# Kernel optimization log

Hardware: AMD Instinct MI355X
Metric: run time of the kernel (lower is better)

## Reference

```python
import jax, jax.numpy as jnp
import numpy as np

NH = 8  # num_heads
CHUNK = 32  # query-block size for chunked L1 cdist


def _mlp(x, w1, b1, w2, b2, w3, b3):
    h = jax.nn.relu(x @ w1 + b1)
    h = jax.nn.relu(h @ w2 + b2)
    return h @ w3 + b3


def _split_heads(x, nh):
    # Faithful to source: reshape last dim as (d, nh) then permute -> [B, nh, S, d]
    B, S, H = x.shape
    return jnp.transpose(x.reshape(B, S, H // nh, nh), (0, 3, 1, 2))


def _cdist_l1(K, Q, chunk=CHUNK):
    # torch.cdist(K, Q, p=1): D[b,h,i,j] = sum_d |K[b,h,i,d] - Q[b,h,j,d]|
    # Chunk over query rows to bound the broadcasted |K-Q| intermediate.
    B, h, Sq, d = Q.shape
    Sk = K.shape[2]
    Qb = jnp.moveaxis(Q.reshape(B, h, Sq // chunk, chunk, d), 2, 0)  # [nb,B,h,chunk,d]

    def block(q):  # q: [B,h,chunk,d]
        return jnp.sum(jnp.abs(K[:, :, :, None, :] - q[:, :, None, :, :]), axis=-1)  # [B,h,Sk,chunk]

    D = jax.lax.map(block, Qb)  # [nb,B,h,Sk,chunk]
    return jnp.moveaxis(D, 0, 3).reshape(B, h, Sk, Sq)


def setup_inputs() -> dict:
    key = jax.random.key(0)
    ks = jax.random.split(key, 32)
    B, S, F, H, O = 4, 1024, 128, 512, 128
    s = 0.02

    def lin(i, fin, fout):
        return (jax.random.normal(ks[i], (fin, fout), jnp.float32) * s,
                jnp.zeros((fout,), jnp.float32))

    inp = {
        'KEY': jax.random.normal(ks[0], (B, S, F), jnp.float32),
        'VALUE': jax.random.normal(ks[1], (B, S, F), jnp.float32),
        'QUERY': jax.random.normal(ks[2], (B, S, F), jnp.float32),
    }
    idx = 3
    for n in ['k', 'q', 'v']:
        for li, (fin, fout) in enumerate([(F, H), (H, H), (H, H)], 1):
            w, b = lin(idx, fin, fout); idx += 1
            inp[f'W{n}_w{li}'] = w
            inp[f'W{n}_b{li}'] = b
    w, b = lin(idx, H, O)
    inp['Wo_w'] = w
    inp['Wo_b'] = b
    return inp


def reference(KEY, VALUE, QUERY,
              Wk_w1, Wk_b1, Wk_w2, Wk_b2, Wk_w3, Wk_b3,
              Wq_w1, Wq_b1, Wq_w2, Wq_b2, Wq_w3, Wq_b3,
              Wv_w1, Wv_b1, Wv_w2, Wv_b2, Wv_w3, Wv_b3,
              Wo_w, Wo_b):
    Wk = _split_heads(_mlp(KEY, Wk_w1, Wk_b1, Wk_w2, Wk_b2, Wk_w3, Wk_b3), NH)   # [B,h,Sk,d]
    Wq = _split_heads(_mlp(QUERY, Wq_w1, Wq_b1, Wq_w2, Wq_b2, Wq_w3, Wq_b3), NH)  # [B,h,Sq,d]
    Wv = _split_heads(_mlp(VALUE, Wv_w1, Wv_b1, Wv_w2, Wv_b2, Wv_w3, Wv_b3), NH)  # [B,h,Sk,d]

    D = _cdist_l1(Wk, Wq)                              # [B,h,Sk,Sq]
    attn = jax.nn.softmax(-(D * D) * 0.5, axis=1)      # softmax over HEAD axis, as in source
    out = jnp.einsum('bhik,bhij->bhjk', attn, Wv)      # [B,h,d,Sq]
    B, h, d, Sq = out.shape
    out = jnp.transpose(out, (0, 2, 1, 3)).reshape(B, d * h, Sq)  # [B,hidden,Sq]
    out = jnp.transpose(out, (0, 2, 1))                # [B,Sq,hidden]
    return out @ Wo_w + Wo_b                           # dropout = identity (eval)
```

## Files before the change

kernel.cpp:

```cpp
#include <hip/hip_runtime.h>
#include <hip/hip_bf16.h>
#include <hip/hip_fp16.h>

typedef unsigned short u16;
typedef __attribute__((ext_vector_type(8))) short short8;
typedef __attribute__((ext_vector_type(4))) float floatx4;

#define DEVI static __device__ __forceinline__

DEVI float bf2f(u16 b) { return __uint_as_float(((unsigned)b) << 16); }
DEVI u16 f2bf(float f) {
  __hip_bfloat16 h = __float2bfloat16(f);
  u16 u; __builtin_memcpy(&u, &h, 2); return u;
}
DEVI u16 f2h(float f) {
  __half h = __float2half(f);
  u16 u; __builtin_memcpy(&u, &h, 2); return u;
}

DEVI void async_ld16(const u16* g, u16* l) {
  __builtin_amdgcn_global_load_lds(
      (const __attribute__((address_space(1))) unsigned int*)g,
      (__attribute__((address_space(3))) unsigned int*)l, 16, 0, 0);
}

template <int CTRL>
DEVI float dpp_add_f(float v) {
  int i; __builtin_memcpy(&i, &v, 4);
  int p = __builtin_amdgcn_update_dpp(0, i, CTRL, 0xF, 0xF, false);
  float pv; __builtin_memcpy(&pv, &p, 4);
  return v + pv;
}

DEVI int hperm(int f) { return ((f & 7) << 6) | (f >> 3); }

struct H4 { __half2 a, b, c, d; };
DEVI H4 toH4(const int4 v) { H4 r; __builtin_memcpy(&r, &v, 16); return r; }
DEVI int4 fromH4(const H4 x) { int4 r; __builtin_memcpy(&r, &x, 16); return r; }

struct TransArgs {
  const float* src[10];
  u16* dst[10];
  int R[10];
  int C[10];
};

__global__ __launch_bounds__(256) void transpose_k(TransArgs t) {
  const int z = blockIdx.z;
  const float* __restrict__ src = t.src[z];
  u16* __restrict__ dst = t.dst[z];
  const int R = t.R[z], C = t.C[z];
  const int c0 = blockIdx.x * 32, r0 = blockIdx.y * 32;
  if (c0 >= C || r0 >= R) return;
  __shared__ float tile[32][33];
  const int tx = threadIdx.x & 31, ty = threadIdx.x >> 5;
  for (int i = ty; i < 32; i += 8)
    tile[i][tx] = src[(size_t)(r0 + i) * C + c0 + tx];
  __syncthreads();
  for (int i = ty; i < 32; i += 8) {
    const int f = r0 + tx;
    const int fi = (z == 9) ? hperm(f) : f;
    dst[(size_t)(c0 + i) * R + fi] = f2bf(tile[tx][i]);
  }
}

struct ConvArgs {
  const float* src[3];
  u16* dst[3];
};

__global__ __launch_bounds__(256) void conv_k(ConvArgs c) {
  const int z = blockIdx.z;
  const float* __restrict__ src = c.src[z];
  u16* __restrict__ dst = c.dst[z];
  const size_t i = ((size_t)blockIdx.x * 256 + threadIdx.x) * 8;
  const float4 f0 = *(const float4*)(src + i);
  const float4 f1 = *(const float4*)(src + i + 4);
  u16 tmp[8] = {f2bf(f0.x), f2bf(f0.y), f2bf(f0.z), f2bf(f0.w),
                f2bf(f1.x), f2bf(f1.y), f2bf(f1.z), f2bf(f1.w)};
  int4 t; __builtin_memcpy(&t, tmp, 16);
  *(int4*)(dst + i) = t;
}

struct GemmArgs {
  const u16* A[3];
  const u16* WT[3];
  const float* bias[3];
  void* C[3];
};

__global__ __launch_bounds__(256, 3) void gemm128(GemmArgs ga, int M, int N, int K,
                                                  int relu, int c_mode, int out_perm) {
  const int z = blockIdx.z;
  const u16* __restrict__ A = ga.A[z];
  const u16* __restrict__ WT = ga.WT[z];
  const float* __restrict__ bias = ga.bias[z];
  void* __restrict__ C = ga.C[z];

  __shared__ u16 As[128 * 64];
  __shared__ u16 Bs[128 * 64];

  const int tid = threadIdx.x;
  const int lane = tid & 63;
  const int wave = tid >> 6;
  const int wm = wave >> 1, wn = wave & 1;
  const int mb = blockIdx.y, nb = blockIdx.x;

  floatx4 acc[4][4];
#pragma unroll
  for (int mi = 0; mi < 4; ++mi)
#pragma unroll
    for (int ni = 0; ni < 4; ++ni) acc[mi][ni] = floatx4{0.f, 0.f, 0.f, 0.f};

  const int g = (lane & 7) ^ ((lane >> 3) & 7);
  const int srow = lane >> 3;
  const size_t aRowBase = (size_t)(mb * 128 + wave * 32 + srow) * K + g * 8;
  const size_t bRowBase = (size_t)(nb * 128 + wave * 32 + srow) * K + g * 8;

  for (int k0 = 0; k0 < K; k0 += 64) {
    __syncthreads();
#pragma unroll
    for (int it = 0; it < 4; ++it) {
      async_ld16(A + aRowBase + (size_t)it * 8 * K + k0, As + (wave * 32 + it * 8) * 64);
      async_ld16(WT + bRowBase + (size_t)it * 8 * K + k0, Bs + (wave * 32 + it * 8) * 64);
    }
    __syncthreads();
#pragma unroll
    for (int ks = 0; ks < 2; ++ks) {
      const int phys = ((ks * 4 + (lane >> 4)) ^ (lane & 7)) * 8;
      short8 af[4], bf[4];
#pragma unroll
      for (int i = 0; i < 4; ++i) {
        const int m = wm * 64 + i * 16 + (lane & 15);
        const int n = wn * 64 + i * 16 + (lane & 15);
        af[i] = *(const short8*)(As + m * 64 + phys);
        bf[i] = *(const short8*)(Bs + n * 64 + phys);
      }
#pragma unroll
      for (int mi = 0; mi < 4; ++mi)
#pragma unroll
        for (int ni = 0; ni < 4; ++ni)
          acc[mi][ni] = __builtin_amdgcn_mfma_f32_16x16x32_bf16(af[mi], bf[ni], acc[mi][ni], 0, 0, 0);
    }
  }

#pragma unroll
  for (int mi = 0; mi < 4; ++mi)
#pragma unroll
    for (int ni = 0; ni < 4; ++ni) {
      const int col = nb * 128 + wn * 64 + ni * 16 + (lane & 15);
      const float bv = bias[col];
      const int colw = out_perm ? hperm(col) : col;
      const floatx4 v = acc[mi][ni];
#pragma unroll
      for (int r = 0; r < 4; ++r) {
        const int row = mb * 128 + wm * 64 + mi * 16 + (lane >> 4) * 4 + r;
        float x = v[r] + bv;
        if (relu) x = fmaxf(x, 0.f);
        if (c_mode == 1)      ((float*)C)[(size_t)row * N + colw] = x;
        else if (c_mode == 2) ((u16*)C)[(size_t)row * N + colw] = f2h(x);
        else                  ((u16*)C)[(size_t)row * N + colw] = f2bf(x);
      }
    }
}

__global__ __launch_bounds__(256, 4) void attn_kernel(const u16* __restrict__ Km,
                                                      const u16* __restrict__ Qm,
                                                      const u16* __restrict__ Vm,
                                                      u16* __restrict__ partial) {
  __shared__ alignas(16) u16 lds[4 * 2048];

  const int tid = threadIdx.x;
  const int lane = tid & 63;
  const int wave = tid >> 6;
  const int wid = blockIdx.x * 4 + wave;
  const int qt = wid & 127;
  const int sp = (wid >> 7) & 15;
  const int b = wid >> 11;
  const int j0 = qt * 8;

  const int qg = lane >> 4;
  const int h = (lane >> 1) & 7;
  const int half = lane & 1;

  int grans[4];
#pragma unroll
  for (int pi = 0; pi < 4; ++pi)
    grans[pi] = h * 8 + half * 4 + ((pi + h) & 3);

  H4 Qh[2][4];
#pragma unroll
  for (int qi = 0; qi < 2; ++qi) {
    const u16* qrow = Qm + (size_t)(b * 1024 + j0 + qg + qi * 4) * 512;
#pragma unroll
    for (int pi = 0; pi < 4; ++pi)
      Qh[qi][pi] = toH4(*(const int4*)(qrow + grans[pi] * 8));
  }

  const __half2 z2 = __float2half2_rn(0.f);
  H4 o[2][4];
#pragma unroll
  for (int qi = 0; qi < 2; ++qi)
#pragma unroll
    for (int pi = 0; pi < 4; ++pi) { o[qi][pi].a = z2; o[qi][pi].b = z2; o[qi][pi].c = z2; o[qi][pi].d = z2; }

  const int keyBase = b * 1024 + sp * 64;
  const u16* kbase = Km + (size_t)keyBase * 512;
  const u16* vbase = Vm + (size_t)keyBase * 512;

#pragma unroll 1
  for (int t = 0; t < 64; ++t) {
    const u16* krow = kbase + t * 512;
    const u16* vrow = vbase + t * 512;
    int4 kvi[4], vvi[4];
#pragma unroll
    for (int pi = 0; pi < 4; ++pi) {
      kvi[pi] = *(const int4*)(krow + grans[pi] * 8);
      vvi[pi] = *(const int4*)(vrow + grans[pi] * 8);
    }

    __half2 a0[2], a1[2];
    a0[0] = z2; a1[0] = z2; a0[1] = z2; a1[1] = z2;
#pragma unroll
    for (int pi = 0; pi < 4; ++pi) {
      const H4 k4 = toH4(kvi[pi]);
#pragma unroll
      for (int qi = 0; qi < 2; ++qi) {
        a0[qi] = __hadd2(a0[qi], __habs2(__hsub2(k4.a, Qh[qi][pi].a)));
        a1[qi] = __hadd2(a1[qi], __habs2(__hsub2(k4.b, Qh[qi][pi].b)));
        a0[qi] = __hadd2(a0[qi], __habs2(__hsub2(k4.c, Qh[qi][pi].c)));
        a1[qi] = __hadd2(a1[qi], __habs2(__hsub2(k4.d, Qh[qi][pi].d)));
      }
    }

    __half2 wh[2];
#pragma unroll
    for (int qi = 0; qi < 2; ++qi) {
      const __half2 s2 = __hadd2(a0[qi], a1[qi]);
      float d8p = __half2float(__low2half(s2)) + __half2float(__high2half(s2));
      const float d8 = dpp_add_f<0xB1>(d8p);
      const float e = __expf(-0.5f * d8 * d8);
      float nrm = e;
      nrm = dpp_add_f<0x4E>(nrm);
      nrm = dpp_add_f<0x141>(nrm);
      nrm = dpp_add_f<0x140>(nrm);
      const float w = e * __builtin_amdgcn_rcpf(nrm);
      wh[qi] = __float2half2_rn(w);
    }

#pragma unroll
    for (int pi = 0; pi < 4; ++pi) {
      const H4 v4 = toH4(vvi[pi]);
#pragma unroll
      for (int qi = 0; qi < 2; ++qi) {
        o[qi][pi].a = __hfma2(wh[qi], v4.a, o[qi][pi].a);
        o[qi][pi].b = __hfma2(wh[qi], v4.b, o[qi][pi].b);
        o[qi][pi].c = __hfma2(wh[qi], v4.c, o[qi][pi].c);
        o[qi][pi].d = __hfma2(wh[qi], v4.d, o[qi][pi].d);
      }
    }
  }

  u16* Ew = lds + wave * 2048;
#pragma unroll
  for (int qi = 0; qi < 2; ++qi) {
#pragma unroll
    for (int pi = 0; pi < 4; ++pi)
      *(int4*)(Ew + qg * 512 + grans[pi] * 8) = fromH4(o[qi][pi]);
    asm volatile("s_waitcnt lgkmcnt(0)" ::: "memory");
#pragma unroll
    for (int p = 0; p < 4; ++p) {
      const int4 v = *(const int4*)(Ew + p * 512 + lane * 8);
      u16* dst = partial + (size_t)sp * (4096 * 512) + (size_t)(b * 1024 + j0 + p + qi * 4) * 512;
      *(int4*)(dst + lane * 8) = v;
    }
    asm volatile("s_waitcnt lgkmcnt(0)" ::: "memory");
  }
}

__global__ __launch_bounds__(256) void reduce_k(const u16* __restrict__ p,
                                                u16* __restrict__ out) {
  const size_t i = ((size_t)blockIdx.x * 256 + threadIdx.x) * 8;
  float s[8] = {0.f, 0.f, 0.f, 0.f, 0.f, 0.f, 0.f, 0.f};
#pragma unroll
  for (int sp = 0; sp < 16; ++sp) {
    const int4 t = *(const int4*)(p + (size_t)sp * (4096 * 512) + i);
    const __half* th = reinterpret_cast<const __half*>(&t);
#pragma unroll
    for (int j = 0; j < 8; ++j) s[j] += __half2float(th[j]);
  }
  int4 pk;
  u16* pu = reinterpret_cast<u16*>(&pk);
#pragma unroll
  for (int j = 0; j < 8; ++j) pu[j] = f2bf(s[j]);
  *(int4*)(out + i) = pk;
}

extern "C" void kernel_launch(void* const* d_in, const int* in_sizes, int n_in,
                              void* d_out, int out_size, void* d_ws, size_t ws_size,
                              hipStream_t stream) {
  (void)in_sizes; (void)n_in; (void)out_size; (void)ws_size;
  char* wsp = (char*)d_ws;
  size_t off = 0;
  auto take = [&](size_t bytes) {
    void* p = (void*)(wsp + off);
    off += ((bytes + 255) & ~(size_t)255);
    return p;
  };

  static const int wR[10] = {128, 512, 512, 128, 512, 512, 128, 512, 512, 512};
  static const int wC[10] = {512, 512, 512, 512, 512, 512, 512, 512, 512, 128};
  static const int widx[10] = {3, 5, 7, 9, 11, 13, 15, 17, 19, 21};

  u16* WT[10];
  for (int i = 0; i < 10; ++i) WT[i] = (u16*)take((size_t)wR[i] * wC[i] * 2);
  u16* a0[3]; for (int i = 0; i < 3; ++i) a0[i] = (u16*)take((size_t)4096 * 128 * 2);
  u16* h1[3]; for (int i = 0; i < 3; ++i) h1[i] = (u16*)take((size_t)4096 * 512 * 2);
  u16* h2[3]; for (int i = 0; i < 3; ++i) h2[i] = (u16*)take((size_t)4096 * 512 * 2);
  u16* partial = (u16*)take((size_t)16 * 4096 * 512 * 2);

  TransArgs ta;
  for (int i = 0; i < 10; ++i) {
    ta.src[i] = (const float*)d_in[widx[i]];
    ta.dst[i] = WT[i];
    ta.R[i] = wR[i];
    ta.C[i] = wC[i];
  }
  hipLaunchKernelGGL(transpose_k, dim3(16, 16, 10), dim3(256), 0, stream, ta);

  ConvArgs ca;
  ca.src[0] = (const float*)d_in[0]; ca.src[1] = (const float*)d_in[2]; ca.src[2] = (const float*)d_in[1];
  ca.dst[0] = a0[0]; ca.dst[1] = a0[1]; ca.dst[2] = a0[2];
  hipLaunchKernelGGL(conv_k, dim3(256, 1, 3), dim3(256), 0, stream, ca);

  GemmArgs g1 = {};
  for (int i = 0; i < 3; ++i) g1.A[i] = a0[i];
  g1.WT[0] = WT[0]; g1.WT[1] = WT[3]; g1.WT[2] = WT[6];
  g1.bias[0] = (const float*)d_in[4]; g1.bias[1] = (const float*)d_in[10]; g1.bias[2] = (const float*)d_in[16];
  g1.C[0] = h1[0]; g1.C[1] = h1[1]; g1.C[2] = h1[2];
  hipLaunchKernelGGL(gemm128, dim3(4, 32, 3), dim3(256), 0, stream, g1, 4096, 512, 128, 1, 0, 0);

  GemmArgs g2 = {};
  for (int i = 0; i < 3; ++i) { g2.A[i] = h1[i]; g2.C[i] = h2[i]; }
  g2.WT[0] = WT[1]; g2.WT[1] = WT[4]; g2.WT[2] = WT[7];
  g2.bias[0] = (const float*)d_in[6]; g2.bias[1] = (const float*)d_in[12]; g2.bias[2] = (const float*)d_in[18];
  hipLaunchKernelGGL(gemm128, dim3(4, 32, 3), dim3(256), 0, stream, g2, 4096, 512, 512, 1, 0, 0);

  GemmArgs g3 = {};
  for (int i = 0; i < 3; ++i) { g3.A[i] = h2[i]; g3.C[i] = (void*)h1[i]; }
  g3.WT[0] = WT[2]; g3.WT[1] = WT[5]; g3.WT[2] = WT[8];
  g3.bias[0] = (const float*)d_in[8]; g3.bias[1] = (const float*)d_in[14]; g3.bias[2] = (const float*)d_in[20];
  hipLaunchKernelGGL(gemm128, dim3(4, 32, 3), dim3(256), 0, stream, g3, 4096, 512, 512, 0, 2, 1);

  hipLaunchKernelGGL(attn_kernel, dim3(2048), dim3(256), 0, stream, h1[0], h1[1], h1[2], partial);

  hipLaunchKernelGGL(reduce_k, dim3(1024), dim3(256), 0, stream, partial, h2[0]);

  GemmArgs g4 = {};
  g4.A[0] = h2[0]; g4.WT[0] = WT[9]; g4.bias[0] = (const float*)d_in[22]; g4.C[0] = d_out;
  hipLaunchKernelGGL(gemm128, dim3(1, 32, 1), dim3(256), 0, stream, g4, 4096, 128, 512, 0, 1, 0);
}
```

Before: 424.3 us.

## Double-buffer K/V rows into LDS with async global-to-LDS loads

The attention kernel now streams K and V rows into a per-wave double-buffered LDS region using global_load_lds, prefetching the next pair of key rows while the current pair is computed, then reads operands from LDS. Previously each iteration issued direct global loads into registers, exposing their latency each step. The change doubles LDS per block, which may reduce occupancy, and adds a vmcnt(0) wait per two keys. There is no explicit sync between the previous iteration's LDS reads and the overwrite of the other buffer, which relies on in-wave ordering.

```diff
diff --git a/kernel.cpp b/kernel.cpp
--- a/kernel.cpp
+++ b/kernel.cpp
@@ -168,7 +168,7 @@
                                                       const u16* __restrict__ Qm,
                                                       const u16* __restrict__ Vm,
                                                       u16* __restrict__ partial) {
-  __shared__ alignas(16) u16 lds[4 * 2048];
+  __shared__ alignas(16) u16 lds[4 * 4096];
 
   const int tid = threadIdx.x;
   const int lane = tid & 63;
@@ -205,63 +205,80 @@
     for (int pi = 0; pi < 4; ++pi) { o[qi][pi].a = z2; o[qi][pi].b = z2; o[qi][pi].c = z2; o[qi][pi].d = z2; }
 
   const int keyBase = b * 1024 + sp * 64;
-  const u16* kbase = Km + (size_t)keyBase * 512;
-  const u16* vbase = Vm + (size_t)keyBase * 512;
+  const u16* kgb = Km + (size_t)keyBase * 512 + lane * 8;
+  const u16* vgb = Vm + (size_t)keyBase * 512 + lane * 8;
+  u16* wbase = lds + wave * 4096;
+
+  async_ld16(kgb, wbase);
+  async_ld16(kgb + 512, wbase + 512);
+  async_ld16(vgb, wbase + 1024);
+  async_ld16(vgb + 512, wbase + 1536);
 
 #pragma unroll 1
-  for (int t = 0; t < 64; ++t) {
-    const u16* krow = kbase + t * 512;
-    const u16* vrow = vbase + t * 512;
-    int4 kvi[4], vvi[4];
-#pragma unroll
-    for (int pi = 0; pi < 4; ++pi) {
-      kvi[pi] = *(const int4*)(krow + grans[pi] * 8);
-      vvi[pi] = *(const int4*)(vrow + grans[pi] * 8);
-    }
-
-    __half2 a0[2], a1[2];
-    a0[0] = z2; a1[0] = z2; a0[1] = z2; a1[1] = z2;
-#pragma unroll
-    for (int pi = 0; pi < 4; ++pi) {
-      const H4 k4 = toH4(kvi[pi]);
+  for (int cc = 0; cc < 32; ++cc) {
+    asm volatile("s_waitcnt vmcnt(0)" ::: "memory");
+    __builtin_amdgcn_sched_barrier(0);
+    const int cur = cc & 1;
+    const u16* buf = wbase + cur * 2048;
+    if (cc < 31) {
+      const u16* kg = kgb + (size_t)(cc + 1) * 1024;
+      const u16* vg = vgb + (size_t)(cc + 1) * 1024;
+      u16* nb = wbase + (cur ^ 1) * 2048;
+      async_ld16(kg, nb);
+      async_ld16(kg + 512, nb + 512);
+      async_ld16(vg, nb + 1024);
+      async_ld16(vg + 512, nb + 1536);
+    }
+
+#pragma unroll
+    for (int r = 0; r < 2; ++r) {
+      const u16* krow = buf + r * 512;
+      const u16* vrow = buf + 1024 + r * 512;
+
+      __half2 a0[2], a1[2];
+      a0[0] = z2; a1[0] = z2; a0[1] = z2; a1[1] = z2;
+#pragma unroll
+      for (int pi = 0; pi < 4; ++pi) {
+        const H4 k4 = toH4(*(const int4*)(krow + grans[pi] * 8));
+#pragma unroll
+        for (int qi = 0; qi < 2; ++qi) {
+          a0[qi] = __hadd2(a0[qi], __habs2(__hsub2(k4.a, Qh[qi][pi].a)));
+          a1[qi] = __hadd2(a1[qi], __habs2(__hsub2(k4.b, Qh[qi][pi].b)));
+          a0[qi] = __hadd2(a0[qi], __habs2(__hsub2(k4.c, Qh[qi][pi].c)));
+          a1[qi] = __hadd2(a1[qi], __habs2(__hsub2(k4.d, Qh[qi][pi].d)));
+        }
+      }
+
+      __half2 wh[2];
 #pragma unroll
       for (int qi = 0; qi < 2; ++qi) {
-        a0[qi] = __hadd2(a0[qi], __habs2(__hsub2(k4.a, Qh[qi][pi].a)));
-        a1[qi] = __hadd2(a1[qi], __habs2(__hsub2(k4.b, Qh[qi][pi].b)));
-        a0[qi] = __hadd2(a0[qi], __habs2(__hsub2(k4.c, Qh[qi][pi].c)));
-        a1[qi] = __hadd2(a1[qi], __habs2(__hsub2(k4.d, Qh[qi][pi].d)));
-      }
-    }
-
-    __half2 wh[2];
-#pragma unroll
-    for (int qi = 0; qi < 2; ++qi) {
-      const __half2 s2 = __hadd2(a0[qi], a1[qi]);
-      float d8p = __half2float(__low2half(s2)) + __half2float(__high2half(s2));
-      const float d8 = dpp_add_f<0xB1>(d8p);
-      const float e = __expf(-0.5f * d8 * d8);
-      float nrm = e;
-      nrm = dpp_add_f<0x4E>(nrm);
-      nrm = dpp_add_f<0x141>(nrm);
-      nrm = dpp_add_f<0x140>(nrm);
-      const float w = e * __builtin_amdgcn_rcpf(nrm);
-      wh[qi] = __float2half2_rn(w);
-    }
-
-#pragma unroll
-    for (int pi = 0; pi < 4; ++pi) {
-      const H4 v4 = toH4(vvi[pi]);
-#pragma unroll
-      for (int qi = 0; qi < 2; ++qi) {
-        o[qi][pi].a = __hfma2(wh[qi], v4.a, o[qi][pi].a);
-        o[qi][pi].b = __hfma2(wh[qi], v4.b, o[qi][pi].b);
-        o[qi][pi].c = __hfma2(wh[qi], v4.c, o[qi][pi].c);
-        o[qi][pi].d = __hfma2(wh[qi], v4.d, o[qi][pi].d);
-      }
-    }
-  }
-
-  u16* Ew = lds + wave * 2048;
+        const __half2 s2 = __hadd2(a0[qi], a1[qi]);
+        float d8p = __half2float(__low2half(s2)) + __half2float(__high2half(s2));
+        const float d8 = dpp_add_f<0xB1>(d8p);
+        const float e = __expf(-0.5f * d8 * d8);
+        float nrm = e;
+        nrm = dpp_add_f<0x4E>(nrm);
+        nrm = dpp_add_f<0x141>(nrm);
+        nrm = dpp_add_f<0x140>(nrm);
+        const float w = e * __builtin_amdgcn_rcpf(nrm);
+        wh[qi] = __float2half2_rn(w);
+      }
+
+#pragma unroll
+      for (int pi = 0; pi < 4; ++pi) {
+        const H4 v4 = toH4(*(const int4*)(vrow + grans[pi] * 8));
+#pragma unroll
+        for (int qi = 0; qi < 2; ++qi) {
+          o[qi][pi].a = __hfma2(wh[qi], v4.a, o[qi][pi].a);
+          o[qi][pi].b = __hfma2(wh[qi], v4.b, o[qi][pi].b);
+          o[qi][pi].c = __hfma2(wh[qi], v4.c, o[qi][pi].c);
+          o[qi][pi].d = __hfma2(wh[qi], v4.d, o[qi][pi].d);
+        }
+      }
+    }
+  }
+
+  u16* Ew = wbase;
 #pragma unroll
   for (int qi = 0; qi < 2; ++qi) {
 #pragma unroll
```

Result: faster. 362.2 us (-14.7%).

## Stage shared K/V rows in LDS with double-buffered async loads across waves

Applied to the files above, without the earlier changes.

The four waves of a block share the same batch and key split, so the K and V rows are now fetched once per block. Each wave issues one async global-to-LDS load per chunk of two key rows, into a double buffer, and all waves then read K and V from LDS. Before, every wave loaded the same rows from global memory into registers, so this removes redundant global and cache traffic. In exchange it adds a block-wide barrier every two keys, enlarges LDS, and raises the launch-bounds occupancy hint from 4 to 6 blocks. The barrier may not wait on the outstanding async LDS load, which is a correctness risk.

```diff
diff --git a/kernel.cpp b/kernel.cpp
--- a/kernel.cpp
+++ b/kernel.cpp
@@ -164,11 +164,11 @@
     }
 }
 
-__global__ __launch_bounds__(256, 4) void attn_kernel(const u16* __restrict__ Km,
+__global__ __launch_bounds__(256, 6) void attn_kernel(const u16* __restrict__ Km,
                                                       const u16* __restrict__ Qm,
                                                       const u16* __restrict__ Vm,
                                                       u16* __restrict__ partial) {
-  __shared__ alignas(16) u16 lds[4 * 2048];
+  __shared__ alignas(16) u16 lds[12288];
 
   const int tid = threadIdx.x;
   const int lane = tid & 63;
@@ -205,63 +205,71 @@
     for (int pi = 0; pi < 4; ++pi) { o[qi][pi].a = z2; o[qi][pi].b = z2; o[qi][pi].c = z2; o[qi][pi].d = z2; }
 
   const int keyBase = b * 1024 + sp * 64;
-  const u16* kbase = Km + (size_t)keyBase * 512;
-  const u16* vbase = Vm + (size_t)keyBase * 512;
+  const u16* srcBase = (wave < 2) ? Km : Vm;
+  const int rowSel = wave & 1;
+  const u16* srcLane = srcBase + (size_t)(keyBase + rowSel) * 512 + lane * 8;
+
+  async_ld16(srcLane, lds + wave * 512);
+  __syncthreads();
 
 #pragma unroll 1
-  for (int t = 0; t < 64; ++t) {
-    const u16* krow = kbase + t * 512;
-    const u16* vrow = vbase + t * 512;
-    int4 kvi[4], vvi[4];
-#pragma unroll
-    for (int pi = 0; pi < 4; ++pi) {
-      kvi[pi] = *(const int4*)(krow + grans[pi] * 8);
-      vvi[pi] = *(const int4*)(vrow + grans[pi] * 8);
-    }
-
-    __half2 a0[2], a1[2];
-    a0[0] = z2; a1[0] = z2; a0[1] = z2; a1[1] = z2;
-#pragma unroll
-    for (int pi = 0; pi < 4; ++pi) {
-      const H4 k4 = toH4(kvi[pi]);
+  for (int c = 0; c < 32; ++c) {
+    const int cur = c & 1;
+    if (c < 31)
+      async_ld16(srcLane + (size_t)(c + 1) * 1024 * 512 / 512,
+                 lds + (cur ^ 1) * 2048 + wave * 512);
+
+    const u16* buf = lds + cur * 2048;
+#pragma unroll
+    for (int r = 0; r < 2; ++r) {
+      const u16* krow = buf + r * 512;
+      const u16* vrow = buf + 1024 + r * 512;
+
+      __half2 a0[2], a1[2];
+      a0[0] = z2; a1[0] = z2; a0[1] = z2; a1[1] = z2;
+#pragma unroll
+      for (int pi = 0; pi < 4; ++pi) {
+        const H4 k4 = toH4(*(const int4*)(krow + grans[pi] * 8));
+#pragma unroll
+        for (int qi = 0; qi < 2; ++qi) {
+          a0[qi] = __hadd2(a0[qi], __habs2(__hsub2(k4.a, Qh[qi][pi].a)));
+          a1[qi] = __hadd2(a1[qi], __habs2(__hsub2(k4.b, Qh[qi][pi].b)));
+          a0[qi] = __hadd2(a0[qi], __habs2(__hsub2(k4.c, Qh[qi][pi].c)));
+          a1[qi] = __hadd2(a1[qi], __habs2(__hsub2(k4.d, Qh[qi][pi].d)));
+        }
+      }
+
+      __half2 wh[2];
 #pragma unroll
       for (int qi = 0; qi < 2; ++qi) {
-        a0[qi] = __hadd2(a0[qi], __habs2(__hsub2(k4.a, Qh[qi][pi].a)));
-        a1[qi] = __hadd2(a1[qi], __habs2(__hsub2(k4.b, Qh[qi][pi].b)));
-        a0[qi] = __hadd2(a0[qi], __habs2(__hsub2(k4.c, Qh[qi][pi].c)));
-        a1[qi] = __hadd2(a1[qi], __habs2(__hsub2(k4.d, Qh[qi][pi].d)));
-      }
-    }
-
-    __half2 wh[2];
-#pragma unroll
-    for (int qi = 0; qi < 2; ++qi) {
-      const __half2 s2 = __hadd2(a0[qi], a1[qi]);
-      float d8p = __half2float(__low2half(s2)) + __half2float(__high2half(s2));
-      const float d8 = dpp_add_f<0xB1>(d8p);
-      const float e = __expf(-0.5f * d8 * d8);
-      float nrm = e;
-      nrm = dpp_add_f<0x4E>(nrm);
-      nrm = dpp_add_f<0x141>(nrm);
-      nrm = dpp_add_f<0x140>(nrm);
-      const float w = e * __builtin_amdgcn_rcpf(nrm);
-      wh[qi] = __float2half2_rn(w);
-    }
-
-#pragma unroll
-    for (int pi = 0; pi < 4; ++pi) {
-      const H4 v4 = toH4(vvi[pi]);
-#pragma unroll
-      for (int qi = 0; qi < 2; ++qi) {
-        o[qi][pi].a = __hfma2(wh[qi], v4.a, o[qi][pi].a);
-        o[qi][pi].b = __hfma2(wh[qi], v4.b, o[qi][pi].b);
-        o[qi][pi].c = __hfma2(wh[qi], v4.c, o[qi][pi].c);
-        o[qi][pi].d = __hfma2(wh[qi], v4.d, o[qi][pi].d);
-      }
-    }
-  }
-
-  u16* Ew = lds + wave * 2048;
+        const __half2 s2 = __hadd2(a0[qi], a1[qi]);
+        float d8p = __half2float(__low2half(s2)) + __half2float(__high2half(s2));
+        const float d8 = dpp_add_f<0xB1>(d8p);
+        const float e = __expf(-0.5f * d8 * d8);
+        float nrm = e;
+        nrm = dpp_add_f<0x4E>(nrm);
+        nrm = dpp_add_f<0x141>(nrm);
+        nrm = dpp_add_f<0x140>(nrm);
+        const float w = e * __builtin_amdgcn_rcpf(nrm);
+        wh[qi] = __float2half2_rn(w);
+      }
+
+#pragma unroll
+      for (int pi = 0; pi < 4; ++pi) {
+        const H4 v4 = toH4(*(const int4*)(vrow + grans[pi] * 8));
+#pragma unroll
+        for (int qi = 0; qi < 2; ++qi) {
+          o[qi][pi].a = __hfma2(wh[qi], v4.a, o[qi][pi].a);
+          o[qi][pi].b = __hfma2(wh[qi], v4.b, o[qi][pi].b);
+          o[qi][pi].c = __hfma2(wh[qi], v4.c, o[qi][pi].c);
+          o[qi][pi].d = __hfma2(wh[qi], v4.d, o[qi][pi].d);
+        }
+      }
+    }
+    __syncthreads();
+  }
+
+  u16* Ew = lds + 4096 + wave * 2048;
 #pragma unroll
   for (int qi = 0; qi < 2; ++qi) {
 #pragma unroll
```

After: 368.6 us. -13.1%, faster.
